# Optimization experiments

Hardware: AMD Instinct MI355X
Metric: run time of the kernel (lower is better)

The kernel has to match this reference:

```python
import jax, jax.numpy as jnp
import numpy as np

T, B, IN, H, L, A = 512, 128, 544, 512, 2, 18


def setup_inputs() -> dict:
    key = jax.random.key(0)
    ks = jax.random.split(key, 16)
    s = 0.02
    return {
        "x": jax.random.normal(ks[0], (T, B, IN), jnp.float32),
        "done": jax.random.randint(ks[1], (T, B), 0, 2, jnp.int32),
        "h0": jax.random.normal(ks[2], (L, B, H), jnp.float32),
        "c0": jax.random.normal(ks[3], (L, B, H), jnp.float32),
        "W_ih0": s * jax.random.normal(ks[4], (4 * H, IN), jnp.float32),
        "W_hh0": s * jax.random.normal(ks[5], (4 * H, H), jnp.float32),
        "b_ih0": jnp.zeros((4 * H,), jnp.float32),
        "b_hh0": jnp.zeros((4 * H,), jnp.float32),
        "W_ih1": s * jax.random.normal(ks[6], (4 * H, H), jnp.float32),
        "W_hh1": s * jax.random.normal(ks[7], (4 * H, H), jnp.float32),
        "b_ih1": jnp.zeros((4 * H,), jnp.float32),
        "b_hh1": jnp.zeros((4 * H,), jnp.float32),
        "W_actor": 0.01 * jax.random.normal(ks[8], (A, H), jnp.float32),
        "b_actor": jnp.zeros((A,), jnp.float32),
        "W_critic": jax.random.normal(ks[9], (1, H), jnp.float32),
        "b_critic": jnp.zeros((1,), jnp.float32),
    }


def _lstm_cell(x, h, c, W_ih, W_hh, b_ih, b_hh):
    # PyTorch gate order: i, f, g, o
    gates = x @ W_ih.T + b_ih + h @ W_hh.T + b_hh  # [B, 4H]
    i, f, g, o = jnp.split(gates, 4, axis=-1)
    c_new = jax.nn.sigmoid(f) * c + jax.nn.sigmoid(i) * jnp.tanh(g)
    h_new = jax.nn.sigmoid(o) * jnp.tanh(c_new)
    return h_new, c_new


def reference(x, done, h0, c0, W_ih0, W_hh0, b_ih0, b_hh0,
              W_ih1, W_hh1, b_ih1, b_hh1, W_actor, b_actor, W_critic, b_critic):
    layer_params = [(W_ih0, W_hh0, b_ih0, b_hh0), (W_ih1, W_hh1, b_ih1, b_hh1)]
    done_f = done.astype(x.dtype)  # [T, B]

    def step(carry, inp):
        h, c = carry                       # each [L, B, H]
        x_t, d_t = inp                     # [B, IN], [B]
        mask = (1.0 - d_t)[None, :, None]  # reset state at episode boundary
        h = h * mask
        c = c * mask
        layer_in = x_t
        hs, cs = [], []
        for l, (Wih, Whh, bih, bhh) in enumerate(layer_params):
            h_l, c_l = _lstm_cell(layer_in, h[l], c[l], Wih, Whh, bih, bhh)
            hs.append(h_l)
            cs.append(c_l)
            layer_in = h_l
        return (jnp.stack(hs), jnp.stack(cs)), layer_in

    (h_T, c_T), hidden = jax.lax.scan(step, (h0, c0), (x, done_f))  # hidden: [T, B, H]
    hidden = hidden.reshape(-1, hidden.shape[-1])                    # [T*B, H]
    logits = hidden @ W_actor.T + b_actor                            # [T*B, A]
    value = hidden @ W_critic.T + b_critic                           # [T*B, 1]
    out = jnp.concatenate([logits, value], axis=-1)                  # [T*B, A+1]
    return out, h_T, c_T
```

## Files before the change

### kernel.cpp

```cpp
#include <hip/hip_runtime.h>
#include <hip/hip_bf16.h>


namespace {
constexpr int T = 512, B = 128, H = 512, NA = 18;
constexpr int BH = B * H;
constexpr int OUT_COLS = NA + 1;
constexpr int OUT_HT = T * B * OUT_COLS;
constexpr int OUT_CT = OUT_HT + 2 * BH;
}

using f32x4 = __attribute__((ext_vector_type(4))) float;
using s16x8 = __attribute__((ext_vector_type(8))) short;

__device__ __forceinline__ unsigned short f2bu(float f) {
  union { __hip_bfloat16 h; unsigned short u; } cv;
  cv.h = __float2bfloat16(f);
  return cv.u;
}
__device__ __forceinline__ float sigm(float x) { return 1.0f / (1.0f + __expf(-x)); }
__device__ __forceinline__ float tanh_f(float x) { return 1.0f - 2.0f / (1.0f + __expf(2.0f * x)); }

__device__ __forceinline__ void spin_group(const unsigned int* f, unsigned int tgt) {
  const unsigned int* p = f + (threadIdx.x & 31);
  for (;;) {
    unsigned int v = __hip_atomic_load(p, __ATOMIC_RELAXED, __HIP_MEMORY_SCOPE_AGENT);
    if (__all((int)(v >= tgt))) break;
    __builtin_amdgcn_s_sleep(1);
  }
}

__device__ __forceinline__ s16x8 ld_frag_agent(const unsigned short* p) {
  const unsigned long long* q = (const unsigned long long*)p;
  unsigned long long a0 = __hip_atomic_load(q, __ATOMIC_RELAXED, __HIP_MEMORY_SCOPE_AGENT);
  unsigned long long a1 = __hip_atomic_load(q + 1, __ATOMIC_RELAXED, __HIP_MEMORY_SCOPE_AGENT);
  union { unsigned long long u[2]; s16x8 v; } r;
  r.u[0] = a0; r.u[1] = a1;
  return r.v;
}

template <int LAYER>
__device__ void lstm_layer(const float* __restrict__ x, const int* __restrict__ done,
                           const float* __restrict__ h0in, const float* __restrict__ c0in,
                           const float* __restrict__ Wih, const float* __restrict__ Whh,
                           const float* __restrict__ bih, const float* __restrict__ bhh,
                           float* __restrict__ out, unsigned short* __restrict__ ring,
                           unsigned short* __restrict__ hist, unsigned int* flags,
                           int bg, int jg, float* red, unsigned short (*hrep)[16][20]) {
  constexpr int NKCMAX = (LAYER == 0) ? 9 : 8;
  const int tid = threadIdx.x;
  const int w = tid >> 6;
  const int lane = tid & 63;
  const int lo = lane & 15;
  const int quad = lane >> 4;
  const int bbase = bg * 32, jbase = jg * 16;
  const bool rec = (w >= 2);

  int kbeg, nkc;
  if (LAYER == 0) { kbeg = (w == 0) ? 0 : (1 + w * 8); nkc = (w == 0) ? 9 : 8; }
  else            { kbeg = w * 8; nkc = 8; }

  s16x8 Bf[4][NKCMAX];
#pragma unroll
  for (int kci = 0; kci < NKCMAX; kci++) {
    if (kci < nkc) {
      int kg = (kbeg + kci) * 32 + quad * 8;
#pragma unroll
      for (int nt = 0; nt < 4; nt++) {
        int row = nt * 512 + jbase + lo;
        const float* src;
        if (LAYER == 0) src = (kg < 544) ? (Wih + row * 544 + kg) : (Whh + row * 512 + (kg - 544));
        else            src = (kg < 512) ? (Wih + row * 512 + kg) : (Whh + row * 512 + (kg - 512));
        union { s16x8 v; unsigned short u[8]; } tu;
#pragma unroll
        for (int j = 0; j < 8; j++) tu.u[j] = f2bu(src[j]);
        Bf[nt][kci] = tu.v;
      }
    }
  }

  float bias[4];
#pragma unroll
  for (int nt = 0; nt < 4; nt++) {
    int row = nt * 512 + jbase + lo;
    bias[nt] = bih[row] + bhh[row];
  }

  const int mt = w & 1;
  const int bE0 = bbase + mt * 16 + quad * 4;
  const int jE = jbase + lo;
  float cst[4] = {0.f, 0.f, 0.f, 0.f};

  unsigned short* slot0 = (LAYER == 0) ? ring : hist;
  if (w < 2) {
#pragma unroll
    for (int r = 0; r < 4; r++) cst[r] = c0in[LAYER * BH + (bE0 + r) * 512 + jE];
    int bI = bbase + mt * 16 + (lane >> 2);
    int jI = jbase + (lane & 3) * 4;
    const float* hp = h0in + LAYER * BH + bI * 512 + jI;
    union { unsigned long long u; unsigned short s[4]; } pk;
#pragma unroll
    for (int j = 0; j < 4; j++) pk.s[j] = f2bu(hp[j]);
    __hip_atomic_store((unsigned long long*)(slot0 + bI * 512 + jI), pk.u,
                       __ATOMIC_RELAXED, __HIP_MEMORY_SCOPE_AGENT);
  }
  __syncthreads();

  const unsigned int* fl0 = flags + (0 + bg) * 32;
  const unsigned int* fl1 = flags + (4 + bg) * 32;
  unsigned int* myflag = (unsigned int*)((LAYER == 0 ? fl0 : fl1) + jg);
  if (tid == 0) {
    __builtin_amdgcn_s_waitcnt(0);
    __hip_atomic_store(myflag, 1u, __ATOMIC_RELAXED, __HIP_MEMORY_SCOPE_AGENT);
  }

  for (int t = 0; t < T; t++) {
    if (LAYER == 0) {
      if (rec) spin_group(fl0, (unsigned)(t + 1));
      else if (t >= 16) spin_group(fl1, (unsigned)(t - 14));
    } else {
      if (rec) spin_group(fl1, (unsigned)(t + 1));
      else     spin_group(fl0, (unsigned)(t + 2));
    }

    const unsigned short* prec[2];
    const unsigned short* pin1[2];
    const float* pxf[2];
    bool dA[2];
#pragma unroll
    for (int m2 = 0; m2 < 2; m2++) {
      int b = bbase + m2 * 16 + lo;
      dA[m2] = rec ? (done[t * B + b] != 0) : false;
      if (LAYER == 0) {
        pxf[m2] = x + (size_t)(t * B + b) * 544 + quad * 8;
        prec[m2] = ring + (t & 15) * BH + b * 512 + quad * 8;
      } else {
        pin1[m2] = ring + ((t + 1) & 15) * BH + b * 512 + quad * 8;
        prec[m2] = hist + (size_t)t * BH + b * 512 + quad * 8;
      }
    }
    const int koff = rec ? (kbeg - (LAYER == 0 ? 17 : 16)) * 32 : kbeg * 32;

    f32x4 acc[2][4];
#pragma unroll
    for (int m2 = 0; m2 < 2; m2++)
#pragma unroll
      for (int nt = 0; nt < 4; nt++) acc[m2][nt] = (f32x4){0.f, 0.f, 0.f, 0.f};

#pragma unroll
    for (int kci = 0; kci < NKCMAX; kci++) {
      if (kci < nkc) {
        int ko = koff + kci * 32;
#pragma unroll
        for (int m2 = 0; m2 < 2; m2++) {
          s16x8 a;
          if (rec) {
            a = ld_frag_agent(prec[m2] + ko);
            if (dA[m2]) a = s16x8{};
          } else if (LAYER == 0) {
            const f32x4* p4 = reinterpret_cast<const f32x4*>(pxf[m2] + ko);
            f32x4 f0 = p4[0], f1 = p4[1];
            union { s16x8 v; unsigned short u[8]; } tu;
#pragma unroll
            for (int j = 0; j < 4; j++) { tu.u[j] = f2bu(f0[j]); tu.u[4 + j] = f2bu(f1[j]); }
            a = tu.v;
          } else {
            a = ld_frag_agent(pin1[m2] + ko);
          }
#pragma unroll
          for (int nt = 0; nt < 4; nt++)
            acc[m2][nt] = __builtin_amdgcn_mfma_f32_16x16x32_bf16(a, Bf[nt][kci], acc[m2][nt], 0, 0, 0);
        }
      }
    }

#pragma unroll
    for (int m2 = 0; m2 < 2; m2++)
#pragma unroll
      for (int nt = 0; nt < 4; nt++)
#pragma unroll
        for (int r = 0; r < 4; r++)
          red[(((w * 2 + m2) * 16) + nt * 4 + r) * 64 + lane] = acc[m2][nt][r];
    __syncthreads();

    if (w < 2) {
      float g[4][4];
#pragma unroll
      for (int nt = 0; nt < 4; nt++)
#pragma unroll
        for (int r = 0; r < 4; r++) {
          int f = nt * 4 + r;
          g[nt][r] = red[((0 * 2 + mt) * 16 + f) * 64 + lane] + red[((1 * 2 + mt) * 16 + f) * 64 + lane] +
                     red[((2 * 2 + mt) * 16 + f) * 64 + lane] + red[((3 * 2 + mt) * 16 + f) * 64 + lane];
        }
      float hnv[4], cnv[4];
#pragma unroll
      for (int r = 0; r < 4; r++) {
        int b = bE0 + r;
        float iv = g[0][r] + bias[0];
        float fv = g[1][r] + bias[1];
        float gv = g[2][r] + bias[2];
        float ov = g[3][r] + bias[3];
        float cp = (done[t * B + b] != 0) ? 0.0f : cst[r];
        float cn = sigm(fv) * cp + sigm(iv) * tanh_f(gv);
        float hn = sigm(ov) * tanh_f(cn);
        cst[r] = cn; hnv[r] = hn; cnv[r] = cn;
        hrep[mt][quad * 4 + r][lo] = f2bu(hn);
      }
      int b2 = lane >> 2, j0l = (lane & 3) * 4;
      unsigned long long pv = *(const unsigned long long*)&hrep[mt][b2][j0l];
      int bS = bbase + mt * 16 + b2, jS = jbase + j0l;
      unsigned short* dstbase = (LAYER == 0) ? (ring + ((t + 1) & 15) * BH)
                                             : (hist + (size_t)(t + 1) * BH);
      __hip_atomic_store((unsigned long long*)(dstbase + bS * 512 + jS), pv,
                         __ATOMIC_RELAXED, __HIP_MEMORY_SCOPE_AGENT);
      if (t == T - 1) {
#pragma unroll
        for (int r = 0; r < 4; r++) {
          int b = bE0 + r;
          out[OUT_HT + LAYER * BH + b * 512 + jE] = hnv[r];
          out[OUT_CT + LAYER * BH + b * 512 + jE] = cnv[r];
        }
      }
    }
    __syncthreads();
    if (tid == 0) {
      __builtin_amdgcn_s_waitcnt(0);
      __hip_atomic_store(myflag, (unsigned)(t + 2), __ATOMIC_RELAXED, __HIP_MEMORY_SCOPE_AGENT);
    }
  }
}

__global__ __launch_bounds__(256, 1) void lstm_persist(
    const float* x, const int* done, const float* h0in, const float* c0in,
    const float* Wih0, const float* Whh0, const float* bih0, const float* bhh0,
    const float* Wih1, const float* Whh1, const float* bih1, const float* bhh1,
    float* out, unsigned short* ring, unsigned short* hist, unsigned int* flags) {
  __shared__ float red[8192];
  __shared__ unsigned short hrep[2][16][20];
  const int bid = blockIdx.x;
  const int layer = bid >> 7;
  const int bl = bid & 127;
  const int bg = bl >> 5, jg = bl & 31;
  if (layer == 0)
    lstm_layer<0>(x, done, h0in, c0in, Wih0, Whh0, bih0, bhh0, out, ring, hist, flags, bg, jg, red, hrep);
  else
    lstm_layer<1>(x, done, h0in, c0in, Wih1, Whh1, bih1, bhh1, out, ring, hist, flags, bg, jg, red, hrep);
}

__global__ __launch_bounds__(256) void head_kernel(const unsigned short* __restrict__ hidden,
                                                   const float* __restrict__ Wa, const float* __restrict__ ba,
                                                   const float* __restrict__ Wc, const float* __restrict__ bc,
                                                   float* __restrict__ out) {
  const int tid = threadIdx.x, w = tid >> 6, lane = tid & 63, lo = lane & 15, quad = lane >> 4;
  const int mbase = blockIdx.x * 128;
  s16x8 Bf[2][16];
#pragma unroll
  for (int nt = 0; nt < 2; nt++) {
    int row = nt * 16 + lo;
#pragma unroll
    for (int kc = 0; kc < 16; kc++) {
      int kg = kc * 32 + quad * 8;
      union { s16x8 v; unsigned short u[8]; } tu;
      if (row < 18) {
        const float* s = Wa + row * 512 + kg;
#pragma unroll
        for (int j = 0; j < 8; j++) tu.u[j] = f2bu(s[j]);
      } else if (row == 18) {
        const float* s = Wc + kg;
#pragma unroll
        for (int j = 0; j < 8; j++) tu.u[j] = f2bu(s[j]);
      } else {
        tu.v = s16x8{};
      }
      Bf[nt][kc] = tu.v;
    }
  }
  f32x4 acc[2][2];
#pragma unroll
  for (int mi = 0; mi < 2; mi++)
#pragma unroll
    for (int nt = 0; nt < 2; nt++) acc[mi][nt] = (f32x4){0.f, 0.f, 0.f, 0.f};
#pragma unroll
  for (int kc = 0; kc < 16; kc++) {
#pragma unroll
    for (int mi = 0; mi < 2; mi++) {
      int m = mbase + (w * 2 + mi) * 16 + lo;
      s16x8 a = *reinterpret_cast<const s16x8*>(hidden + (size_t)m * 512 + kc * 32 + quad * 8);
      acc[mi][0] = __builtin_amdgcn_mfma_f32_16x16x32_bf16(a, Bf[0][kc], acc[mi][0], 0, 0, 0);
      acc[mi][1] = __builtin_amdgcn_mfma_f32_16x16x32_bf16(a, Bf[1][kc], acc[mi][1], 0, 0, 0);
    }
  }
  float b0 = ba[lo];
  float b1 = (lo < 2) ? ba[16 + lo] : ((lo == 2) ? bc[0] : 0.f);
#pragma unroll
  for (int mi = 0; mi < 2; mi++)
#pragma unroll
    for (int r = 0; r < 4; r++) {
      int m = mbase + (w * 2 + mi) * 16 + quad * 4 + r;
      out[(size_t)m * 19 + lo] = acc[mi][0][r] + b0;
      if (lo < 3) out[(size_t)m * 19 + 16 + lo] = acc[mi][1][r] + b1;
    }
}

extern "C" void kernel_launch(void* const* d_in, const int* in_sizes, int n_in,
                              void* d_out, int out_size, void* d_ws, size_t ws_size,
                              hipStream_t stream) {
  const float* x = (const float*)d_in[0];
  const int* done = (const int*)d_in[1];
  const float* h0 = (const float*)d_in[2];
  const float* c0 = (const float*)d_in[3];
  const float* Wih0 = (const float*)d_in[4];
  const float* Whh0 = (const float*)d_in[5];
  const float* bih0 = (const float*)d_in[6];
  const float* bhh0 = (const float*)d_in[7];
  const float* Wih1 = (const float*)d_in[8];
  const float* Whh1 = (const float*)d_in[9];
  const float* bih1 = (const float*)d_in[10];
  const float* bhh1 = (const float*)d_in[11];
  const float* Wa = (const float*)d_in[12];
  const float* ba = (const float*)d_in[13];
  const float* Wc = (const float*)d_in[14];
  const float* bc = (const float*)d_in[15];
  float* out = (float*)d_out;

  char* ws = (char*)d_ws;
  unsigned int* flags = (unsigned int*)ws;
  unsigned short* ring = (unsigned short*)(ws + 4096);
  unsigned short* hist = (unsigned short*)(ws + 4096 + 16 * 65536 * 2);

  hipMemsetAsync(flags, 0, 4096, stream);
  lstm_persist<<<dim3(256), dim3(256), 0, stream>>>(
      x, done, h0, c0, Wih0, Whh0, bih0, bhh0, Wih1, Whh1, bih1, bhh1,
      out, ring, hist, flags);
  head_kernel<<<dim3(512), dim3(256), 0, stream>>>(hist + 65536, Wa, ba, Wc, bc, out);
}
```

Before: 6.636 ms.

## Replace per-block flag polling with per-timestep arrival counters and full history buffers

```diff
diff --git a/kernel.cpp b/kernel.cpp
--- a/kernel.cpp
+++ b/kernel.cpp
@@ -21,12 +21,11 @@
 __device__ __forceinline__ float sigm(float x) { return 1.0f / (1.0f + __expf(-x)); }
 __device__ __forceinline__ float tanh_f(float x) { return 1.0f - 2.0f / (1.0f + __expf(2.0f * x)); }
 
-__device__ __forceinline__ void spin_group(const unsigned int* f, unsigned int tgt) {
-  const unsigned int* p = f + (threadIdx.x & 31);
+__device__ __forceinline__ void poll32(unsigned int* p) {
   for (;;) {
-    unsigned int v = __hip_atomic_load(p, __ATOMIC_RELAXED, __HIP_MEMORY_SCOPE_AGENT);
-    if (__all((int)(v >= tgt))) break;
-    __builtin_amdgcn_s_sleep(1);
+    unsigned int v = __hip_atomic_fetch_add(p, 0u, __ATOMIC_RELAXED, __HIP_MEMORY_SCOPE_AGENT);
+    if (v >= 32u) return;
+    __builtin_amdgcn_s_sleep(4);
   }
 }
 
@@ -39,13 +38,22 @@
   return r.v;
 }
 
+__device__ __forceinline__ s16x8 cvt8(const float* p) {
+  const f32x4* q = (const f32x4*)p;
+  f32x4 a = q[0], b = q[1];
+  union { s16x8 v; unsigned short u[8]; } t;
+#pragma unroll
+  for (int j = 0; j < 4; j++) { t.u[j] = f2bu(a[j]); t.u[4 + j] = f2bu(b[j]); }
+  return t.v;
+}
+
 template <int LAYER>
 __device__ void lstm_layer(const float* __restrict__ x, const int* __restrict__ done,
                            const float* __restrict__ h0in, const float* __restrict__ c0in,
                            const float* __restrict__ Wih, const float* __restrict__ Whh,
                            const float* __restrict__ bih, const float* __restrict__ bhh,
-                           float* __restrict__ out, unsigned short* __restrict__ ring,
-                           unsigned short* __restrict__ hist, unsigned int* flags,
+                           float* __restrict__ out, unsigned short* __restrict__ h0h,
+                           unsigned short* __restrict__ h1h, unsigned int* cnt,
                            int bg, int jg, float* red, unsigned short (*hrep)[16][20]) {
   constexpr int NKCMAX = (LAYER == 0) ? 9 : 8;
   const int tid = threadIdx.x;
@@ -69,12 +77,9 @@
       for (int nt = 0; nt < 4; nt++) {
         int row = nt * 512 + jbase + lo;
         const float* src;
-        if (LAYER == 0) src = (kg < 544) ? (Wih + row * 544 + kg) : (Whh + row * 512 + (kg - 544));
-        else            src = (kg < 512) ? (Wih + row * 512 + kg) : (Whh + row * 512 + (kg - 512));
-        union { s16x8 v; unsigned short u[8]; } tu;
-#pragma unroll
-        for (int j = 0; j < 8; j++) tu.u[j] = f2bu(src[j]);
-        Bf[nt][kci] = tu.v;
+        if (LAYER == 0) src = (kg < 544) ? (Wih + (size_t)row * 544 + kg) : (Whh + (size_t)row * 512 + (kg - 544));
+        else            src = (kg < 512) ? (Wih + (size_t)row * 512 + kg) : (Whh + (size_t)row * 512 + (kg - 512));
+        Bf[nt][kci] = cvt8(src);
       }
     }
   }
@@ -91,7 +96,7 @@
   const int jE = jbase + lo;
   float cst[4] = {0.f, 0.f, 0.f, 0.f};
 
-  unsigned short* slot0 = (LAYER == 0) ? ring : hist;
+  unsigned short* myh = (LAYER == 0) ? h0h : h1h;
   if (w < 2) {
 #pragma unroll
     for (int r = 0; r < 4; r++) cst[r] = c0in[LAYER * BH + (bE0 + r) * 512 + jE];
@@ -101,27 +106,29 @@
     union { unsigned long long u; unsigned short s[4]; } pk;
 #pragma unroll
     for (int j = 0; j < 4; j++) pk.s[j] = f2bu(hp[j]);
-    __hip_atomic_store((unsigned long long*)(slot0 + bI * 512 + jI), pk.u,
+    __hip_atomic_store((unsigned long long*)(myh + bI * 512 + jI), pk.u,
                        __ATOMIC_RELAXED, __HIP_MEMORY_SCOPE_AGENT);
   }
   __syncthreads();
 
-  const unsigned int* fl0 = flags + (0 + bg) * 32;
-  const unsigned int* fl1 = flags + (4 + bg) * 32;
-  unsigned int* myflag = (unsigned int*)((LAYER == 0 ? fl0 : fl1) + jg);
+  unsigned int* c0a = cnt + (0 * 4 + bg) * 1024;
+  unsigned int* c1a = cnt + (1 * 4 + bg) * 1024;
+  unsigned int* cmy = (LAYER == 0) ? c0a : c1a;
   if (tid == 0) {
     __builtin_amdgcn_s_waitcnt(0);
-    __hip_atomic_store(myflag, 1u, __ATOMIC_RELAXED, __HIP_MEMORY_SCOPE_AGENT);
+    __hip_atomic_fetch_add(cmy + 0, 1u, __ATOMIC_RELAXED, __HIP_MEMORY_SCOPE_AGENT);
   }
 
   for (int t = 0; t < T; t++) {
-    if (LAYER == 0) {
-      if (rec) spin_group(fl0, (unsigned)(t + 1));
-      else if (t >= 16) spin_group(fl1, (unsigned)(t - 14));
-    } else {
-      if (rec) spin_group(fl1, (unsigned)(t + 1));
-      else     spin_group(fl0, (unsigned)(t + 2));
-    }
+    if (tid == 0) {
+      if (LAYER == 0) {
+        poll32(c0a + t);
+      } else {
+        poll32(c1a + t);
+        poll32(c0a + t + 1);
+      }
+    }
+    __syncthreads();
 
     const unsigned short* prec[2];
     const unsigned short* pin1[2];
@@ -133,10 +140,10 @@
       dA[m2] = rec ? (done[t * B + b] != 0) : false;
       if (LAYER == 0) {
         pxf[m2] = x + (size_t)(t * B + b) * 544 + quad * 8;
-        prec[m2] = ring + (t & 15) * BH + b * 512 + quad * 8;
+        prec[m2] = h0h + (size_t)t * BH + b * 512 + quad * 8;
       } else {
-        pin1[m2] = ring + ((t + 1) & 15) * BH + b * 512 + quad * 8;
-        prec[m2] = hist + (size_t)t * BH + b * 512 + quad * 8;
+        pin1[m2] = h0h + (size_t)(t + 1) * BH + b * 512 + quad * 8;
+        prec[m2] = h1h + (size_t)t * BH + b * 512 + quad * 8;
       }
     }
     const int koff = rec ? (kbeg - (LAYER == 0 ? 17 : 16)) * 32 : kbeg * 32;
@@ -158,12 +165,7 @@
             a = ld_frag_agent(prec[m2] + ko);
             if (dA[m2]) a = s16x8{};
           } else if (LAYER == 0) {
-            const f32x4* p4 = reinterpret_cast<const f32x4*>(pxf[m2] + ko);
-            f32x4 f0 = p4[0], f1 = p4[1];
-            union { s16x8 v; unsigned short u[8]; } tu;
-#pragma unroll
-            for (int j = 0; j < 4; j++) { tu.u[j] = f2bu(f0[j]); tu.u[4 + j] = f2bu(f1[j]); }
-            a = tu.v;
+            a = cvt8(pxf[m2] + ko);
           } else {
             a = ld_frag_agent(pin1[m2] + ko);
           }
@@ -210,9 +212,7 @@
       int b2 = lane >> 2, j0l = (lane & 3) * 4;
       unsigned long long pv = *(const unsigned long long*)&hrep[mt][b2][j0l];
       int bS = bbase + mt * 16 + b2, jS = jbase + j0l;
-      unsigned short* dstbase = (LAYER == 0) ? (ring + ((t + 1) & 15) * BH)
-                                             : (hist + (size_t)(t + 1) * BH);
-      __hip_atomic_store((unsigned long long*)(dstbase + bS * 512 + jS), pv,
+      __hip_atomic_store((unsigned long long*)(myh + (size_t)(t + 1) * BH + bS * 512 + jS), pv,
                          __ATOMIC_RELAXED, __HIP_MEMORY_SCOPE_AGENT);
       if (t == T - 1) {
 #pragma unroll
@@ -226,7 +226,7 @@
     __syncthreads();
     if (tid == 0) {
       __builtin_amdgcn_s_waitcnt(0);
-      __hip_atomic_store(myflag, (unsigned)(t + 2), __ATOMIC_RELAXED, __HIP_MEMORY_SCOPE_AGENT);
+      __hip_atomic_fetch_add(cmy + (t + 1), 1u, __ATOMIC_RELAXED, __HIP_MEMORY_SCOPE_AGENT);
     }
   }
 }
@@ -235,7 +235,7 @@
     const float* x, const int* done, const float* h0in, const float* c0in,
     const float* Wih0, const float* Whh0, const float* bih0, const float* bhh0,
     const float* Wih1, const float* Whh1, const float* bih1, const float* bhh1,
-    float* out, unsigned short* ring, unsigned short* hist, unsigned int* flags) {
+    float* out, unsigned short* h0h, unsigned short* h1h, unsigned int* cnt) {
   __shared__ float red[8192];
   __shared__ unsigned short hrep[2][16][20];
   const int bid = blockIdx.x;
@@ -243,9 +243,9 @@
   const int bl = bid & 127;
   const int bg = bl >> 5, jg = bl & 31;
   if (layer == 0)
-    lstm_layer<0>(x, done, h0in, c0in, Wih0, Whh0, bih0, bhh0, out, ring, hist, flags, bg, jg, red, hrep);
+    lstm_layer<0>(x, done, h0in, c0in, Wih0, Whh0, bih0, bhh0, out, h0h, h1h, cnt, bg, jg, red, hrep);
   else
-    lstm_layer<1>(x, done, h0in, c0in, Wih1, Whh1, bih1, bhh1, out, ring, hist, flags, bg, jg, red, hrep);
+    lstm_layer<1>(x, done, h0in, c0in, Wih1, Whh1, bih1, bhh1, out, h0h, h1h, cnt, bg, jg, red, hrep);
 }
 
 __global__ __launch_bounds__(256) void head_kernel(const unsigned short* __restrict__ hidden,
@@ -325,13 +325,17 @@
   float* out = (float*)d_out;
 
   char* ws = (char*)d_ws;
-  unsigned int* flags = (unsigned int*)ws;
-  unsigned short* ring = (unsigned short*)(ws + 4096);
-  unsigned short* hist = (unsigned short*)(ws + 4096 + 16 * 65536 * 2);
-
-  hipMemsetAsync(flags, 0, 4096, stream);
+  const size_t cntBytes = 32768;
+  const size_t h0Off = cntBytes;
+  const size_t h1Off = h0Off + (size_t)(T + 1) * BH * 2;
+
+  unsigned int* cnt = (unsigned int*)ws;
+  unsigned short* h0h = (unsigned short*)(ws + h0Off);
+  unsigned short* h1h = (unsigned short*)(ws + h1Off);
+
+  hipMemsetAsync(cnt, 0, cntBytes, stream);
   lstm_persist<<<dim3(256), dim3(256), 0, stream>>>(
       x, done, h0, c0, Wih0, Whh0, bih0, bhh0, Wih1, Whh1, bih1, bhh1,
-      out, ring, hist, flags);
-  head_kernel<<<dim3(512), dim3(256), 0, stream>>>(hist + 65536, Wa, ba, Wc, bc, out);
-}
+      out, h0h, h1h, cnt);
+  head_kernel<<<dim3(512), dim3(256), 0, stream>>>(h1h + BH, Wa, ba, Wc, bc, out);
+}
```

After: 7.517 ms. 1.13x slower.
